# Performance work log

Measured on AMD Instinct MI355X. Metric: run time of the kernel, lower is better.

The kernel has to match this reference:

```python
import jax, jax.numpy as jnp
import numpy as np

C = 32  # input multiplicity per irrep (0e and 1o)
D = 32  # output multiplicity per irrep


def pe_inputs(x):
    # x: [B, 2, 3, F]; permutation-equivariant pooled channels
    x_self = x
    x_flavor = x.sum(axis=2, keepdims=True) - x_self
    x_nunubar = x.sum(axis=1, keepdims=True) - x_self
    x_all = x.sum(axis=(1, 2), keepdims=True) - x_self - x_flavor - x_nunubar
    x_flavor = x_flavor / (x.shape[2] - 1)
    x_nunubar = x_nunubar / (x.shape[1] - 1)
    x_all = x_all / ((x.shape[1] - 1) * (x.shape[2] - 1))
    return x_self, x_flavor, x_nunubar, x_all


def _split(x):
    # irreps '32x0e + 32x1o': first C scalars, then C vectors flattened (C,3)
    s = x[..., :C]
    v = x[..., C:].reshape(x.shape[:-1] + (C, 3))
    return s, v


def fctp(x1, x2, W):
    # e3nn FullyConnectedTensorProduct('Cx0e+Cx1o', 'Cx0e+Cx1o', 'Dx0e+Dx1o')
    # W: [4, C, C, D] stacked path weights: [ss->s, vv->s, sv->v, vs->v]
    s1, v1 = _split(x1)
    s2, v2 = _split(x2)
    norm = 1.0 / (C * np.sqrt(2.0))  # sqrt(dim(ir_out) / fan), fan = 2*C^2
    inv_sqrt3 = 1.0 / np.sqrt(3.0)   # wigner_3j(1,1,0) = delta_ij/sqrt(3)
    y_s = norm * (jnp.einsum('uvw,...u,...v->...w', W[0], s1, s2)
                  + inv_sqrt3 * jnp.einsum('uvw,...ui,...vi->...w', W[1], v1, v2))
    y_v = norm * (jnp.einsum('uvw,...u,...vk->...wk', W[2], s1, v2)
                  + jnp.einsum('uvw,...uk,...v->...wk', W[3], v1, s2))
    return jnp.concatenate([y_s, y_v.reshape(y_v.shape[:-2] + (3 * D,))], axis=-1)


def setup_inputs() -> dict:
    key = jax.random.key(0)
    ks = jax.random.split(key, 5)
    B = 16384
    x = jax.random.normal(ks[0], (B, 2, 3, C + 3 * C), dtype=jnp.float32)
    W_self = jax.random.normal(ks[1], (4, C, C, D), dtype=jnp.float32)
    W_flavor = jax.random.normal(ks[2], (4, C, C, D), dtype=jnp.float32)
    W_nunubar = jax.random.normal(ks[3], (4, C, C, D), dtype=jnp.float32)
    W_all = jax.random.normal(ks[4], (4, C, C, D), dtype=jnp.float32)
    return {"x": x, "W_self": W_self, "W_flavor": W_flavor,
            "W_nunubar": W_nunubar, "W_all": W_all}


def reference(x, W_self, W_flavor, W_nunubar, W_all):
    xs, xf, xn, xa = pe_inputs(x)
    y = (fctp(xs, xs, W_self)
         + fctp(xf, xf, W_flavor)
         + fctp(xn, xn, W_nunubar)
         + fctp(xa, xa, W_all))
    return y
```

## Files before the change

### kernel.cpp

```cpp
#include <hip/hip_runtime.h>


typedef _Float16 half8 __attribute__((ext_vector_type(8)));
typedef float   float4_t __attribute__((ext_vector_type(4)));

#define NORM 0.022097086912079608f
#define INV_SQRT3 0.5773502691896258f
#define FS 194

__global__ void prep_kernel(const float* __restrict__ Wa, const float* __restrict__ Wb,
                            const float* __restrict__ Wc, const float* __restrict__ Wd,
                            _Float16* __restrict__ B1s, _Float16* __restrict__ B2s) {
    const float* Ws[4] = {Wa, Wb, Wc, Wd};
    int idx = blockIdx.x * 256 + threadIdx.x;
    if (idx < 262144) {
        int j    = idx & 7;
        int lane = (idx >> 3) & 63;
        int h    = (idx >> 9) & 1;
        int s    = (idx >> 10) & 3;
        int ch   = (idx >> 12) & 15;
        int t    = idx >> 16;
        int m = lane & 15, q = lane >> 4;
        int n = h * 16 + m;
        int k = ch * 128 + s * 32 + q * 8 + j;
        int seg = k >> 10, u = (k >> 5) & 31, v = k & 31;
        const float* W = Ws[t];
        float val;
        if (seg == 0) val = NORM * W[0 * 32768 + u * 1024 + v * 32 + n];
        else          val = NORM * INV_SQRT3 * W[1 * 32768 + u * 1024 + v * 32 + n];
        B1s[idx] = (_Float16)val;
    } else {
        int idx2 = idx - 262144;
        if (idx2 < 131072) {
            int j    = idx2 & 7;
            int lane = (idx2 >> 3) & 63;
            int h    = (idx2 >> 9) & 1;
            int s2   = (idx2 >> 10) & 1;
            int ch   = (idx2 >> 11) & 15;
            int t    = idx2 >> 15;
            int m = lane & 15, q = lane >> 4;
            int n = h * 16 + m;
            int k = ch * 64 + s2 * 32 + q * 8 + j;
            int u = k >> 5, v = k & 31;
            const float* W = Ws[t];
            float val = NORM * (W[2 * 32768 + u * 1024 + v * 32 + n] +
                                W[3 * 32768 + v * 1024 + u * 32 + n]);
            B2s[idx2] = (_Float16)val;
        }
    }
}

__launch_bounds__(256, 2)
__global__ void petp_main(const float* __restrict__ x,
                          const _Float16* __restrict__ B1s,
                          const _Float16* __restrict__ B2s,
                          float* __restrict__ y) {
    __shared__ _Float16 featT[128 * FS];

    const int tid  = threadIdx.x;
    const int wave = tid >> 6;
    const int lane = tid & 63;
    const int m = lane & 15;
    const int q = lane >> 4;
    const int wg = blockIdx.x;
    const int pbase = wave * 48;

    float4_t acc_s[3][2];
    float4_t acc_v[9][2];
    float4_t zero = {0.f, 0.f, 0.f, 0.f};
#pragma unroll
    for (int i = 0; i < 3; ++i) { acc_s[i][0] = zero; acc_s[i][1] = zero; }
#pragma unroll
    for (int i = 0; i < 9; ++i) { acc_v[i][0] = zero; acc_v[i][1] = zero; }

    const float* xg = x + (size_t)wg * (192 * 128);

#pragma unroll 1
    for (int t = 0; t < 4; ++t) {
        __syncthreads();
#pragma unroll 1
        for (int it = 0; it < 16; ++it) {
            int item = it * 256 + tid;
            int b = item >> 7;
            int c = item & 127;
            const float* bp = xg + b * 768 + c;
            float v00 = bp[0],   v01 = bp[128], v02 = bp[256];
            float v10 = bp[384], v11 = bp[512], v12 = bp[640];
            float rs0 = v00 + v01 + v02, rs1 = v10 + v11 + v12;
            float cs0 = v00 + v10, cs1 = v01 + v11, cs2 = v02 + v12;
            float tot = rs0 + rs1;
            float xv[6] = {v00, v01, v02, v10, v11, v12};
            float rs[2] = {rs0, rs1};
            float cs[3] = {cs0, cs1, cs2};
            int row;
            if (c < 32) row = c;
            else { int cc = c - 32; row = 32 + (cc % 3) * 32 + (cc / 3); }
#pragma unroll
            for (int p6 = 0; p6 < 6; ++p6) {
                int i = p6 / 3, j = p6 % 3;
                float xvv = xv[p6];
                float f;
                if      (t == 0) f = xvv;
                else if (t == 1) f = (rs[i] - xvv) * 0.5f;
                else if (t == 2) f = cs[j] - xvv;
                else             f = (tot - rs[i] - cs[j] + xvv) * 0.5f;
                int posL = b * 6 + p6;
                featT[row * FS + posL] = (_Float16)f;
            }
        }
        __syncthreads();

        half8 p_ss[3];
        half8 p_v[3][3];
#pragma unroll
        for (int tl = 0; tl < 3; ++tl) {
            int posL = pbase + tl * 16 + m;
#pragma unroll
            for (int j = 0; j < 8; ++j)
                p_ss[tl][j] = featT[(q * 8 + j) * FS + posL];
#pragma unroll
            for (int i = 0; i < 3; ++i)
#pragma unroll
                for (int j = 0; j < 8; ++j)
                    p_v[tl][i][j] = featT[(32 + i * 32 + q * 8 + j) * FS + posL];
        }

        const _Float16* B1w = B1s + t * 65536 + lane * 8;
        const _Float16* B2w = B2s + t * 32768 + lane * 8;

#pragma unroll 1
        for (int ch = 0; ch < 16; ++ch) {
            half8 b1f[2][4];
            half8 b2f[2][2];
#pragma unroll
            for (int s = 0; s < 4; ++s) {
                b1f[0][s] = *(const half8*)(B1w + ((ch * 4 + s) * 2 + 0) * 512);
                b1f[1][s] = *(const half8*)(B1w + ((ch * 4 + s) * 2 + 1) * 512);
            }
#pragma unroll
            for (int s2 = 0; s2 < 2; ++s2) {
                b2f[0][s2] = *(const half8*)(B2w + ((ch * 2 + s2) * 2 + 0) * 512);
                b2f[1][s2] = *(const half8*)(B2w + ((ch * 2 + s2) * 2 + 1) * 512);
            }

            if (ch < 8) {
#pragma unroll
                for (int s = 0; s < 4; ++s) {
                    int u = ch * 4 + s;
#pragma unroll
                    for (int tl = 0; tl < 3; ++tl) {
                        int posL = pbase + tl * 16 + m;
                        _Float16 bc = featT[u * FS + posL];
                        half8 af = p_ss[tl] * bc;
                        acc_s[tl][0] = __builtin_amdgcn_mfma_f32_16x16x32_f16(af, b1f[0][s], acc_s[tl][0], 0, 0, 0);
                        acc_s[tl][1] = __builtin_amdgcn_mfma_f32_16x16x32_f16(af, b1f[1][s], acc_s[tl][1], 0, 0, 0);
                    }
                }
            } else {
#pragma unroll
                for (int s = 0; s < 4; ++s) {
                    int u = (ch - 8) * 4 + s;
#pragma unroll
                    for (int tl = 0; tl < 3; ++tl) {
                        int posL = pbase + tl * 16 + m;
                        _Float16 g0 = featT[(32 + u) * FS + posL];
                        _Float16 g1 = featT[(64 + u) * FS + posL];
                        _Float16 g2 = featT[(96 + u) * FS + posL];
                        half8 af = p_v[tl][0] * g0 + p_v[tl][1] * g1 + p_v[tl][2] * g2;
                        acc_s[tl][0] = __builtin_amdgcn_mfma_f32_16x16x32_f16(af, b1f[0][s], acc_s[tl][0], 0, 0, 0);
                        acc_s[tl][1] = __builtin_amdgcn_mfma_f32_16x16x32_f16(af, b1f[1][s], acc_s[tl][1], 0, 0, 0);
                    }
                }
            }
#pragma unroll
            for (int s2 = 0; s2 < 2; ++s2) {
                int u = ch * 2 + s2;
                _Float16 bcs[3];
#pragma unroll
                for (int sub = 0; sub < 3; ++sub)
                    bcs[sub] = featT[u * FS + pbase + sub * 16 + m];
#pragma unroll
                for (int tv = 0; tv < 9; ++tv) {
                    int sub = tv % 3, kc = tv / 3;
                    half8 af = p_v[sub][kc] * bcs[sub];
                    acc_v[tv][0] = __builtin_amdgcn_mfma_f32_16x16x32_f16(af, b2f[0][s2], acc_v[tv][0], 0, 0, 0);
                    acc_v[tv][1] = __builtin_amdgcn_mfma_f32_16x16x32_f16(af, b2f[1][s2], acc_v[tv][1], 0, 0, 0);
                }
            }
        }
    }

    float* yg = y + (size_t)wg * (192 * 128);
#pragma unroll
    for (int tl = 0; tl < 3; ++tl) {
#pragma unroll
        for (int nh = 0; nh < 2; ++nh) {
            int w = nh * 16 + m;
#pragma unroll
            for (int r = 0; r < 4; ++r) {
                int pos = wave * 48 + tl * 16 + q * 4 + r;
                yg[pos * 128 + w] = acc_s[tl][nh][r];
            }
        }
    }
#pragma unroll
    for (int tv = 0; tv < 9; ++tv) {
        int sub = tv % 3, kc = tv / 3;
#pragma unroll
        for (int nh = 0; nh < 2; ++nh) {
            int w = nh * 16 + m;
#pragma unroll
            for (int r = 0; r < 4; ++r) {
                int pos = wave * 48 + sub * 16 + q * 4 + r;
                yg[pos * 128 + 32 + 3 * w + kc] = acc_v[tv][nh][r];
            }
        }
    }
}

extern "C" void kernel_launch(void* const* d_in, const int* in_sizes, int n_in,
                              void* d_out, int out_size, void* d_ws, size_t ws_size,
                              hipStream_t stream) {
    const float* x  = (const float*)d_in[0];
    const float* Wa = (const float*)d_in[1];
    const float* Wb = (const float*)d_in[2];
    const float* Wc = (const float*)d_in[3];
    const float* Wd = (const float*)d_in[4];
    float* y = (float*)d_out;

    _Float16* B1s = (_Float16*)d_ws;
    _Float16* B2s = B1s + 262144;

    int nbatch = in_sizes[0] / 768;
    int nwg = nbatch / 32;

    prep_kernel<<<(262144 + 131072) / 256, 256, 0, stream>>>(Wa, Wb, Wc, Wd, B1s, B2s);
    petp_main<<<nwg, 256, 0, stream>>>(x, B1s, B2s, y);
}
```

Measured before the change: 233.8 us.

## Switch to 32x32x16 MFMA with position-major LDS layout and smaller workgroups

Replaces the 16x16x32 MFMA tiling with 32x32x16 MFMA, so each wave computes 32 positions by 32 outputs using one scalar accumulator and three vector accumulators. The shared feature tile is stored position-major with stride 136, which allows vectorized half8 LDS reads instead of scalar gathers. Weight pre-swizzling is reordered to match the new fragment layout. Workgroups shrink to 192 threads handling 16 batches, with launch bounds allowing three blocks per CU. Per-u weight fragments are now loaded from global memory inside the inner loop, which may increase load pressure.

```diff
diff --git a/kernel.cpp b/kernel.cpp
--- a/kernel.cpp
+++ b/kernel.cpp
@@ -1,12 +1,12 @@
 #include <hip/hip_runtime.h>
 
 
-typedef _Float16 half8 __attribute__((ext_vector_type(8)));
-typedef float   float4_t __attribute__((ext_vector_type(4)));
+typedef _Float16 half8  __attribute__((ext_vector_type(8)));
+typedef float    f32x16 __attribute__((ext_vector_type(16)));
 
 #define NORM 0.022097086912079608f
 #define INV_SQRT3 0.5773502691896258f
-#define FS 194
+#define STR 136
 
 __global__ void prep_kernel(const float* __restrict__ Wa, const float* __restrict__ Wb,
                             const float* __restrict__ Wc, const float* __restrict__ Wd,
@@ -16,32 +16,27 @@
     if (idx < 262144) {
         int j    = idx & 7;
         int lane = (idx >> 3) & 63;
-        int h    = (idx >> 9) & 1;
-        int s    = (idx >> 10) & 3;
-        int ch   = (idx >> 12) & 15;
+        int kh   = (idx >> 9) & 1;
+        int u    = (idx >> 10) & 31;
+        int seg  = (idx >> 15) & 1;
         int t    = idx >> 16;
-        int m = lane & 15, q = lane >> 4;
-        int n = h * 16 + m;
-        int k = ch * 128 + s * 32 + q * 8 + j;
-        int seg = k >> 10, u = (k >> 5) & 31, v = k & 31;
+        int n = lane & 31;
+        int v = kh * 16 + (lane >> 5) * 8 + j;
         const float* W = Ws[t];
         float val;
-        if (seg == 0) val = NORM * W[0 * 32768 + u * 1024 + v * 32 + n];
-        else          val = NORM * INV_SQRT3 * W[1 * 32768 + u * 1024 + v * 32 + n];
+        if (seg == 0) val = NORM * W[u * 1024 + v * 32 + n];
+        else          val = NORM * INV_SQRT3 * W[32768 + u * 1024 + v * 32 + n];
         B1s[idx] = (_Float16)val;
     } else {
         int idx2 = idx - 262144;
         if (idx2 < 131072) {
             int j    = idx2 & 7;
             int lane = (idx2 >> 3) & 63;
-            int h    = (idx2 >> 9) & 1;
-            int s2   = (idx2 >> 10) & 1;
-            int ch   = (idx2 >> 11) & 15;
+            int kh   = (idx2 >> 9) & 1;
+            int u    = (idx2 >> 10) & 31;
             int t    = idx2 >> 15;
-            int m = lane & 15, q = lane >> 4;
-            int n = h * 16 + m;
-            int k = ch * 64 + s2 * 32 + q * 8 + j;
-            int u = k >> 5, v = k & 31;
+            int n = lane & 31;
+            int v = kh * 16 + (lane >> 5) * 8 + j;
             const float* W = Ws[t];
             float val = NORM * (W[2 * 32768 + u * 1024 + v * 32 + n] +
                                 W[3 * 32768 + v * 1024 + u * 32 + n]);
@@ -50,171 +45,130 @@
     }
 }
 
-__launch_bounds__(256, 2)
+__launch_bounds__(192, 3)
 __global__ void petp_main(const float* __restrict__ x,
                           const _Float16* __restrict__ B1s,
                           const _Float16* __restrict__ B2s,
                           float* __restrict__ y) {
-    __shared__ _Float16 featT[128 * FS];
+    __shared__ _Float16 feat[96 * STR];
 
     const int tid  = threadIdx.x;
     const int wave = tid >> 6;
     const int lane = tid & 63;
-    const int m = lane & 15;
-    const int q = lane >> 4;
+    const int mw = lane & 31;
+    const int q8 = lane >> 5;
+
+    f32x16 acc_s;
+    f32x16 acc_v[3];
+#pragma unroll
+    for (int r = 0; r < 16; ++r) {
+        acc_s[r] = 0.f; acc_v[0][r] = 0.f; acc_v[1][r] = 0.f; acc_v[2][r] = 0.f;
+    }
+
     const int wg = blockIdx.x;
-    const int pbase = wave * 48;
-
-    float4_t acc_s[3][2];
-    float4_t acc_v[9][2];
-    float4_t zero = {0.f, 0.f, 0.f, 0.f};
-#pragma unroll
-    for (int i = 0; i < 3; ++i) { acc_s[i][0] = zero; acc_s[i][1] = zero; }
-#pragma unroll
-    for (int i = 0; i < 9; ++i) { acc_v[i][0] = zero; acc_v[i][1] = zero; }
-
-    const float* xg = x + (size_t)wg * (192 * 128);
+    const float* xg = x + (size_t)wg * (96 * 128);
 
 #pragma unroll 1
     for (int t = 0; t < 4; ++t) {
         __syncthreads();
 #pragma unroll 1
-        for (int it = 0; it < 16; ++it) {
-            int item = it * 256 + tid;
-            int b = item >> 7;
-            int c = item & 127;
-            const float* bp = xg + b * 768 + c;
-            float v00 = bp[0],   v01 = bp[128], v02 = bp[256];
-            float v10 = bp[384], v11 = bp[512], v12 = bp[640];
-            float rs0 = v00 + v01 + v02, rs1 = v10 + v11 + v12;
-            float cs0 = v00 + v10, cs1 = v01 + v11, cs2 = v02 + v12;
-            float tot = rs0 + rs1;
-            float xv[6] = {v00, v01, v02, v10, v11, v12};
-            float rs[2] = {rs0, rs1};
-            float cs[3] = {cs0, cs1, cs2};
-            int row;
-            if (c < 32) row = c;
-            else { int cc = c - 32; row = 32 + (cc % 3) * 32 + (cc / 3); }
+        for (int it = 0; it < 11; ++it) {
+            int item = it * 192 + tid;
+            if (item < 2048) {
+                int b = item >> 7;
+                int c = item & 127;
+                const float* bp = xg + b * 768 + c;
+                float v00 = bp[0],   v01 = bp[128], v02 = bp[256];
+                float v10 = bp[384], v11 = bp[512], v12 = bp[640];
+                float rs0 = v00 + v01 + v02, rs1 = v10 + v11 + v12;
+                float cs0 = v00 + v10, cs1 = v01 + v11, cs2 = v02 + v12;
+                float tot = rs0 + rs1;
+                float xv[6] = {v00, v01, v02, v10, v11, v12};
+                float rs[2] = {rs0, rs1};
+                float cs[3] = {cs0, cs1, cs2};
+                int row;
+                if (c < 32) row = c;
+                else { int cc = c - 32; row = 32 + (cc % 3) * 32 + (cc / 3); }
+                _Float16* fp = feat + row;
 #pragma unroll
-            for (int p6 = 0; p6 < 6; ++p6) {
-                int i = p6 / 3, j = p6 % 3;
-                float xvv = xv[p6];
-                float f;
-                if      (t == 0) f = xvv;
-                else if (t == 1) f = (rs[i] - xvv) * 0.5f;
-                else if (t == 2) f = cs[j] - xvv;
-                else             f = (tot - rs[i] - cs[j] + xvv) * 0.5f;
-                int posL = b * 6 + p6;
-                featT[row * FS + posL] = (_Float16)f;
+                for (int p6 = 0; p6 < 6; ++p6) {
+                    int i = p6 / 3, j = p6 % 3;
+                    float xvv = xv[p6];
+                    float f;
+                    if      (t == 0) f = xvv;
+                    else if (t == 1) f = (rs[i] - xvv) * 0.5f;
+                    else if (t == 2) f = cs[j] - xvv;
+                    else             f = (tot - rs[i] - cs[j] + xvv) * 0.5f;
+                    fp[(b * 6 + p6) * STR] = (_Float16)f;
+                }
             }
         }
         __syncthreads();
 
-        half8 p_ss[3];
-        half8 p_v[3][3];
+        const _Float16* frow = feat + (wave * 32 + mw) * STR;
+        half8 sl_s[2];
+        half8 sl_v[2][3];
 #pragma unroll
-        for (int tl = 0; tl < 3; ++tl) {
-            int posL = pbase + tl * 16 + m;
-#pragma unroll
-            for (int j = 0; j < 8; ++j)
-                p_ss[tl][j] = featT[(q * 8 + j) * FS + posL];
+        for (int kh = 0; kh < 2; ++kh) {
+            sl_s[kh] = *(const half8*)(frow + kh * 16 + q8 * 8);
 #pragma unroll
             for (int i = 0; i < 3; ++i)
-#pragma unroll
-                for (int j = 0; j < 8; ++j)
-                    p_v[tl][i][j] = featT[(32 + i * 32 + q * 8 + j) * FS + posL];
+                sl_v[kh][i] = *(const half8*)(frow + 32 + i * 32 + kh * 16 + q8 * 8);
         }
-
-        const _Float16* B1w = B1s + t * 65536 + lane * 8;
-        const _Float16* B2w = B2s + t * 32768 + lane * 8;
+        const _Float16* B1t = B1s + t * 65536 + lane * 8;
+        const _Float16* B2t = B2s + t * 32768 + lane * 8;
 
 #pragma unroll 1
-        for (int ch = 0; ch < 16; ++ch) {
-            half8 b1f[2][4];
-            half8 b2f[2][2];
+        for (int cku = 0; cku < 4; ++cku) {
+            half8 bcS  = *(const half8*)(frow + cku * 8);
+            half8 bcG0 = *(const half8*)(frow + 32 + cku * 8);
+            half8 bcG1 = *(const half8*)(frow + 64 + cku * 8);
+            half8 bcG2 = *(const half8*)(frow + 96 + cku * 8);
 #pragma unroll
-            for (int s = 0; s < 4; ++s) {
-                b1f[0][s] = *(const half8*)(B1w + ((ch * 4 + s) * 2 + 0) * 512);
-                b1f[1][s] = *(const half8*)(B1w + ((ch * 4 + s) * 2 + 1) * 512);
-            }
+            for (int uu = 0; uu < 8; ++uu) {
+                int u = cku * 8 + uu;
+                const _Float16* pA = B1t + u * 1024;
+                const _Float16* pG = B1t + 32768 + u * 1024;
+                const _Float16* pV = B2t + u * 1024;
+                half8 bA0 = *(const half8*)(pA);
+                half8 bA1 = *(const half8*)(pA + 512);
+                half8 bG0 = *(const half8*)(pG);
+                half8 bG1 = *(const half8*)(pG + 512);
+                half8 bV0 = *(const half8*)(pV);
+                half8 bV1 = *(const half8*)(pV + 512);
+                _Float16 su = bcS[uu];
+                _Float16 g0 = bcG0[uu], g1 = bcG1[uu], g2 = bcG2[uu];
+
+                half8 af;
+                af = sl_s[0] * su;
+                acc_s = __builtin_amdgcn_mfma_f32_32x32x16_f16(af, bA0, acc_s, 0, 0, 0);
+                af = sl_s[1] * su;
+                acc_s = __builtin_amdgcn_mfma_f32_32x32x16_f16(af, bA1, acc_s, 0, 0, 0);
+                af = sl_v[0][0] * g0 + sl_v[0][1] * g1 + sl_v[0][2] * g2;
+                acc_s = __builtin_amdgcn_mfma_f32_32x32x16_f16(af, bG0, acc_s, 0, 0, 0);
+                af = sl_v[1][0] * g0 + sl_v[1][1] * g1 + sl_v[1][2] * g2;
+                acc_s = __builtin_amdgcn_mfma_f32_32x32x16_f16(af, bG1, acc_s, 0, 0, 0);
 #pragma unroll
-            for (int s2 = 0; s2 < 2; ++s2) {
-                b2f[0][s2] = *(const half8*)(B2w + ((ch * 2 + s2) * 2 + 0) * 512);
-                b2f[1][s2] = *(const half8*)(B2w + ((ch * 2 + s2) * 2 + 1) * 512);
-            }
-
-            if (ch < 8) {
-#pragma unroll
-                for (int s = 0; s < 4; ++s) {
-                    int u = ch * 4 + s;
-#pragma unroll
-                    for (int tl = 0; tl < 3; ++tl) {
-                        int posL = pbase + tl * 16 + m;
-                        _Float16 bc = featT[u * FS + posL];
-                        half8 af = p_ss[tl] * bc;
-                        acc_s[tl][0] = __builtin_amdgcn_mfma_f32_16x16x32_f16(af, b1f[0][s], acc_s[tl][0], 0, 0, 0);
-                        acc_s[tl][1] = __builtin_amdgcn_mfma_f32_16x16x32_f16(af, b1f[1][s], acc_s[tl][1], 0, 0, 0);
-                    }
-                }
-            } else {
-#pragma unroll
-                for (int s = 0; s < 4; ++s) {
-                    int u = (ch - 8) * 4 + s;
-#pragma unroll
-                    for (int tl = 0; tl < 3; ++tl) {
-                        int posL = pbase + tl * 16 + m;
-                        _Float16 g0 = featT[(32 + u) * FS + posL];
-                        _Float16 g1 = featT[(64 + u) * FS + posL];
-                        _Float16 g2 = featT[(96 + u) * FS + posL];
-                        half8 af = p_v[tl][0] * g0 + p_v[tl][1] * g1 + p_v[tl][2] * g2;
-                        acc_s[tl][0] = __builtin_amdgcn_mfma_f32_16x16x32_f16(af, b1f[0][s], acc_s[tl][0], 0, 0, 0);
-                        acc_s[tl][1] = __builtin_amdgcn_mfma_f32_16x16x32_f16(af, b1f[1][s], acc_s[tl][1], 0, 0, 0);
-                    }
-                }
-            }
-#pragma unroll
-            for (int s2 = 0; s2 < 2; ++s2) {
-                int u = ch * 2 + s2;
-                _Float16 bcs[3];
-#pragma unroll
-                for (int sub = 0; sub < 3; ++sub)
-                    bcs[sub] = featT[u * FS + pbase + sub * 16 + m];
-#pragma unroll
-                for (int tv = 0; tv < 9; ++tv) {
-                    int sub = tv % 3, kc = tv / 3;
-                    half8 af = p_v[sub][kc] * bcs[sub];
-                    acc_v[tv][0] = __builtin_amdgcn_mfma_f32_16x16x32_f16(af, b2f[0][s2], acc_v[tv][0], 0, 0, 0);
-                    acc_v[tv][1] = __builtin_amdgcn_mfma_f32_16x16x32_f16(af, b2f[1][s2], acc_v[tv][1], 0, 0, 0);
+                for (int kc = 0; kc < 3; ++kc) {
+                    half8 af0 = sl_v[0][kc] * su;
+                    acc_v[kc] = __builtin_amdgcn_mfma_f32_32x32x16_f16(af0, bV0, acc_v[kc], 0, 0, 0);
+                    half8 af1 = sl_v[1][kc] * su;
+                    acc_v[kc] = __builtin_amdgcn_mfma_f32_32x32x16_f16(af1, bV1, acc_v[kc], 0, 0, 0);
                 }
             }
         }
     }
 
-    float* yg = y + (size_t)wg * (192 * 128);
+    float* yg = y + (size_t)wg * (96 * 128);
+    const int pb = wave * 32 + q8 * 4;
 #pragma unroll
-    for (int tl = 0; tl < 3; ++tl) {
-#pragma unroll
-        for (int nh = 0; nh < 2; ++nh) {
-            int w = nh * 16 + m;
-#pragma unroll
-            for (int r = 0; r < 4; ++r) {
-                int pos = wave * 48 + tl * 16 + q * 4 + r;
-                yg[pos * 128 + w] = acc_s[tl][nh][r];
-            }
-        }
-    }
-#pragma unroll
-    for (int tv = 0; tv < 9; ++tv) {
-        int sub = tv % 3, kc = tv / 3;
-#pragma unroll
-        for (int nh = 0; nh < 2; ++nh) {
-            int w = nh * 16 + m;
-#pragma unroll
-            for (int r = 0; r < 4; ++r) {
-                int pos = wave * 48 + sub * 16 + q * 4 + r;
-                yg[pos * 128 + 32 + 3 * w + kc] = acc_v[tv][nh][r];
-            }
-        }
+    for (int r = 0; r < 16; ++r) {
+        int pos = pb + (r & 3) + 8 * (r >> 2);
+        float* yp = yg + pos * 128;
+        yp[mw] = acc_s[r];
+        yp[32 + 3 * mw + 0] = acc_v[0][r];
+        yp[32 + 3 * mw + 1] = acc_v[1][r];
+        yp[32 + 3 * mw + 2] = acc_v[2][r];
     }
 }
 
@@ -232,8 +186,8 @@
     _Float16* B2s = B1s + 262144;
 
     int nbatch = in_sizes[0] / 768;
-    int nwg = nbatch / 32;
+    int nwg = nbatch / 16;
 
     prep_kernel<<<(262144 + 131072) / 256, 256, 0, stream>>>(Wa, Wb, Wc, Wd, B1s, B2s);
-    petp_main<<<nwg, 256, 0, stream>>>(x, B1s, B2s, y);
+    petp_main<<<nwg, 192, 0, stream>>>(x, B1s, B2s, y);
 }
```

After: 324.1 us. 1.39x slower.
